# Performance work log

Measured on AMD Instinct MI355X. Metric: run time of the kernel, lower is better.

## Reference

```python
import jax, jax.numpy as jnp
import numpy as np

B, DIN, H, DOUT = 4096, 2048, 4096, 2048


def setup_inputs() -> dict:
    key = jax.random.key(0)
    ks = jax.random.split(key, 17)
    x = jax.random.normal(ks[0], (B, DIN), dtype=jnp.float32)
    W0 = jax.random.randint(ks[1], (H, DIN), -127, 128, dtype=jnp.int32)
    b0 = jax.random.randint(ks[2], (H,), -127, 128, dtype=jnp.int32)
    W2 = jax.random.randint(ks[3], (H, H), -127, 128, dtype=jnp.int32)
    b2 = jax.random.randint(ks[4], (H,), -127, 128, dtype=jnp.int32)
    W4 = jax.random.randint(ks[5], (DOUT, H), -127, 128, dtype=jnp.int32)
    b4 = jax.random.randint(ks[6], (DOUT,), -127, 128, dtype=jnp.int32)
    # amax scalars: positive calibration ranges in [0.5, 2.0)
    amaxes = [jax.random.uniform(ks[7 + i], (), jnp.float32, 0.5, 2.0) for i in range(9)]
    (a0_in, a0_w, a0_b, a2_in, a2_w, a2_b, a4_in, a4_w, a4_b) = amaxes
    return {"x": x, "W0": W0, "b0": b0, "W2": W2, "b2": b2, "W4": W4, "b4": b4,
            "a0_in": a0_in, "a0_w": a0_w, "a0_b": a0_b,
            "a2_in": a2_in, "a2_w": a2_w, "a2_b": a2_b,
            "a4_in": a4_in, "a4_w": a4_w, "a4_b": a4_b}


def _quant(x, amax):
    # torch: clamp(round(x * 127/amax), -127, 127).int()
    scale = 127.0 / amax
    return jnp.clip(jnp.round(x * scale), -127.0, 127.0).astype(jnp.int32)


def _layer(x, W, b, a_in, a_w, a_b):
    xq = _quant(x, a_in)                                      # [B, in] int32
    acc = jnp.matmul(xq, W.T, preferred_element_type=jnp.int32)  # [B, out] int32
    y = acc.astype(jnp.float32) * (a_w * a_in / (127.0 ** 2))    # double dequant
    return y + b.astype(jnp.float32) * (a_b / 127.0)             # single dequant bias


def reference(x, W0, b0, W2, b2, W4, b4,
              a0_in, a0_w, a0_b, a2_in, a2_w, a2_b, a4_in, a4_w, a4_b):
    x = x.reshape(x.shape[0], -1)
    x = _layer(x, W0, b0, a0_in, a0_w, a0_b)
    x = jax.nn.relu(x)
    x = _layer(x, W2, b2, a2_in, a2_w, a2_b)
    x = jax.nn.relu(x)
    x = _layer(x, W4, b4, a4_in, a4_w, a4_b)
    return x
```

## Files before the change

kernel.cpp:

```cpp
#include <hip/hip_runtime.h>

using i32x4 = __attribute__((ext_vector_type(4))) int;

#define DEVI static __device__ __forceinline__

DEVI void gload_lds16(const void* g, void* l) {
  __builtin_amdgcn_global_load_lds(
      (const __attribute__((address_space(1))) void*)g,
      (__attribute__((address_space(3))) void*)l, 16, 0, 0);
}

template <int N> DEVI void vmcnt_n() {
  asm volatile("s_waitcnt vmcnt(%0)" ::"n"(N) : "memory");
}
template <int N> DEVI void lgkm_n() {
  asm volatile("s_waitcnt lgkmcnt(%0)" ::"n"(N) : "memory");
}

#define FENCE() asm volatile("" ::: "memory")
#define BARX()                    \
  do {                            \
    FENCE();                      \
    __builtin_amdgcn_s_barrier(); \
    FENCE();                      \
  } while (0)
#define SCHB() __builtin_amdgcn_sched_barrier(0)
#define PRIO1() __builtin_amdgcn_s_setprio(1)
#define PRIO0() __builtin_amdgcn_s_setprio(0)

__global__ void __launch_bounds__(256) pack_w_kernel(const int* __restrict__ w,
                                                     signed char* __restrict__ o,
                                                     int n4) {
  int stride = gridDim.x * blockDim.x;
  for (int i = blockIdx.x * blockDim.x + threadIdx.x; i < n4; i += stride) {
    int4 v = reinterpret_cast<const int4*>(w)[i];
    char4 c;
    c.x = (signed char)v.x;
    c.y = (signed char)v.y;
    c.z = (signed char)v.z;
    c.w = (signed char)v.w;
    reinterpret_cast<char4*>(o)[i] = c;
  }
}

__global__ void __launch_bounds__(256) quant_x_kernel(const float* __restrict__ x,
                                                      signed char* __restrict__ o,
                                                      const float* __restrict__ amax,
                                                      int n4) {
  const float s = 127.0f / amax[0];
  int stride = gridDim.x * blockDim.x;
  for (int i = blockIdx.x * blockDim.x + threadIdx.x; i < n4; i += stride) {
    float4 v = reinterpret_cast<const float4*>(x)[i];
    char4 c;
    float q;
    q = fminf(fmaxf(rintf(__fmul_rn(v.x, s)), -127.0f), 127.0f); c.x = (signed char)(int)q;
    q = fminf(fmaxf(rintf(__fmul_rn(v.y, s)), -127.0f), 127.0f); c.y = (signed char)(int)q;
    q = fminf(fmaxf(rintf(__fmul_rn(v.z, s)), -127.0f), 127.0f); c.z = (signed char)(int)q;
    q = fminf(fmaxf(rintf(__fmul_rn(v.w, s)), -127.0f), 127.0f); c.w = (signed char)(int)q;
    reinterpret_cast<char4*>(o)[i] = c;
  }
}


#define GB(b, j, k0_)                                           \
  gload_lds16(Wb + (size_t)((j)*64 + srow) * K + (k0_),         \
              &lds[b][ABYTES + (j)*8192 + tid * 16])
#define GA(b, r0, k0_)                                          \
  gload_lds16(Ab + (size_t)((r0) + srow) * K + (k0_),           \
              &lds[b][(r0)*128 + tid * 16])

#define STG_B_EARLY(b, kt)                                              \
  do {                                                                  \
    const int k0_ = (kt)*128 + scol;                                    \
    _Pragma("unroll") for (int j = 0; j < NBE; ++j) GB(b, j, k0_);      \
  } while (0)
#define STG_B_LATE(b, kt)                                               \
  do {                                                                  \
    const int k0_ = (kt)*128 + scol;                                    \
    _Pragma("unroll") for (int j = NBE; j < NN; ++j) GB(b, j, k0_);     \
  } while (0)
#define STG_A01(b, kt)               \
  do {                               \
    const int k0_ = (kt)*128 + scol; \
    GA(b, 0, k0_);                   \
    GA(b, 128, k0_);                 \
  } while (0)
#define STG_A23(b, kt)               \
  do {                               \
    const int k0_ = (kt)*128 + scol; \
    GA(b, 64, k0_);                  \
    GA(b, 192, k0_);                 \
  } while (0)

#define AF_(b, m, h) \
  (*(const i32x4*)&lds[b][(wrl + (m)*16 + ro) * 128 + ((h) ? cS1 : cS0)])
#define BF_(b, n, h) \
  (*(const i32x4*)&lds[b][ABYTES + (wcl + (n)*16 + ro) * 128 + ((h) ? cS1 : cS0)])

#define RD_AF(dst, b, m0)            \
  do {                               \
    dst[0][0] = AF_(b, m0, 0);       \
    dst[0][1] = AF_(b, m0, 1);       \
    dst[1][0] = AF_(b, (m0) + 1, 0); \
    dst[1][1] = AF_(b, (m0) + 1, 1); \
  } while (0)

#define READ_BF(b)                                   \
  do {                                               \
    _Pragma("unroll") for (int n = 0; n < NN; ++n) { \
      bf[n][0] = BF_(b, n, 0);                       \
      bf[n][1] = BF_(b, n, 1);                       \
    }                                                \
  } while (0)

#define MFMA_P(mp, af)                                                                     \
  do {                                                                                     \
    _Pragma("unroll") for (int n = 0; n < NN; ++n) {                                       \
      acc[2 * (mp)][n] =                                                                   \
          __builtin_amdgcn_mfma_i32_16x16x64_i8(af[0][0], bf[n][0], acc[2 * (mp)][n], 0, 0, 0); \
      acc[2 * (mp)][n] =                                                                   \
          __builtin_amdgcn_mfma_i32_16x16x64_i8(af[0][1], bf[n][1], acc[2 * (mp)][n], 0, 0, 0); \
      acc[2 * (mp) + 1][n] = __builtin_amdgcn_mfma_i32_16x16x64_i8(                        \
          af[1][0], bf[n][0], acc[2 * (mp) + 1][n], 0, 0, 0);                              \
      acc[2 * (mp) + 1][n] = __builtin_amdgcn_mfma_i32_16x16x64_i8(                        \
          af[1][1], bf[n][1], acc[2 * (mp) + 1][n], 0, 0, 0);                              \
    }                                                                                      \
  } while (0)

#define TILE_STEADY(b, t)                       \
  do {                                          \
    READ_BF(b);                                 \
    RD_AF(afB, b, 2);                           \
    STG_B_LATE(1 - (b), (t) + 1);               \
    STG_A01(1 - (b), (t) + 1);                  \
    vmcnt_n<NN + 2>();                          \
    BARX(); lgkm_n<4>(); SCHB();                \
    PRIO1(); MFMA_P(0, afA); PRIO0();           \
    RD_AF(afA, b, 4);                           \
    STG_A23(1 - (b), (t) + 1);                  \
    BARX(); lgkm_n<4>(); SCHB();                \
    PRIO1(); MFMA_P(1, afB); PRIO0();           \
    RD_AF(afB, b, 6);                           \
    vmcnt_n<2>();                               \
    BARX(); lgkm_n<4>(); SCHB();                \
    PRIO1(); MFMA_P(2, afA); PRIO0();           \
    RD_AF(afA, 1 - (b), 0);                     \
    if ((t) + 2 < nt) STG_B_EARLY(b, (t) + 2);  \
    BARX(); lgkm_n<4>(); SCHB();                \
    PRIO1(); MFMA_P(3, afB); PRIO0();           \
  } while (0)

#define TILE_LAST(b)                            \
  do {                                          \
    READ_BF(b);                                 \
    RD_AF(afB, b, 2);                           \
    vmcnt_n<0>();                               \
    BARX(); lgkm_n<4>(); SCHB();                \
    PRIO1(); MFMA_P(0, afA); PRIO0();           \
    RD_AF(afA, b, 4);                           \
    BARX(); lgkm_n<4>(); SCHB();                \
    PRIO1(); MFMA_P(1, afB); PRIO0();           \
    RD_AF(afB, b, 6);                           \
    BARX(); lgkm_n<4>(); SCHB();                \
    PRIO1(); MFMA_P(2, afA); PRIO0();           \
    BARX(); lgkm_n<0>(); SCHB();                \
    PRIO1(); MFMA_P(3, afB); PRIO0();           \
  } while (0)

template <int BN, int OUT_I8>
__global__ __launch_bounds__(512, 2) void gemm8_kernel(
    const signed char* __restrict__ A, const signed char* __restrict__ W,
    const int* __restrict__ bias, void* __restrict__ out, int M, int N, int K,
    const float* __restrict__ p_ain, const float* __restrict__ p_aw,
    const float* __restrict__ p_ab, const float* __restrict__ p_anext) {
  static_assert(BN == 256 || BN == 128, "");
  constexpr int NN = BN / 64;
  constexpr int NBE = NN / 2;
  constexpr int ABYTES = 256 * 128;
  __shared__ signed char lds[2][ABYTES + BN * 128];

  const int tid = threadIdx.x;
  const int lane = tid & 63;
  const int wave = tid >> 6;
  const int wrl = (wave >> 2) * 128;
  const int wcl = (wave & 3) * (BN / 4);
  const int tileM = blockIdx.y * 256;
  const int tileN = blockIdx.x * BN;

  const signed char* Ab = A + (size_t)tileM * K;
  const signed char* Wb = W + (size_t)tileN * K;

  const int srow = tid >> 3;
  const int scol = ((tid & 7) ^ (srow & 7)) * 16;

  const int ro = lane & 15;
  const int kg = lane >> 4;
  const int cS0 = ((kg ^ (ro & 7)) << 4);
  const int cS1 = (((4 + kg) ^ (ro & 7)) << 4);

  const int nt = K >> 7;

  i32x4 acc[8][NN] = {};
  i32x4 afA[2][2], afB[2][2], bf[NN][2];

  {
    const int k0_ = scol;
#pragma unroll
    for (int j = 0; j < NN; ++j) GB(0, j, k0_);
    GA(0, 0, k0_);
    GA(0, 128, k0_);
    GA(0, 64, k0_);
    GA(0, 192, k0_);
  }
  FENCE();
  STG_B_EARLY(1, 1);
  vmcnt_n<NBE>();
  BARX();
  RD_AF(afA, 0, 0);

  for (int t = 0; t < nt - 2; t += 2) {
    TILE_STEADY(0, t);
    TILE_STEADY(1, t + 1);
  }
  TILE_STEADY(0, nt - 2);
  TILE_LAST(1);

  const float s1 = __fmul_rn(p_aw[0], p_ain[0]) / 16129.0f;
  const float s2 = p_ab[0] / 127.0f;
  float qs = 0.0f;
  if (OUT_I8) qs = 127.0f / p_anext[0];

#pragma unroll
  for (int m = 0; m < 8; ++m) {
#pragma unroll
    for (int n = 0; n < NN; ++n) {
      const int col = tileN + wcl + n * 16 + ro;
      const int row0 = tileM + wrl + m * 16 + kg * 4;
      const float bv = __fmul_rn((float)bias[col], s2);
#pragma unroll
      for (int i = 0; i < 4; ++i) {
        float y = __fadd_rn(__fmul_rn((float)acc[m][n][i], s1), bv);
        if (OUT_I8) {
          float rl = fmaxf(y, 0.0f);
          float q = fminf(rintf(__fmul_rn(rl, qs)), 127.0f);
          ((signed char*)out)[(size_t)(row0 + i) * N + col] = (signed char)(int)q;
        } else {
          ((float*)out)[(size_t)(row0 + i) * N + col] = y;
        }
      }
    }
  }
}

extern "C" void kernel_launch(void* const* d_in, const int* in_sizes, int n_in,
                              void* d_out, int out_size, void* d_ws, size_t ws_size,
                              hipStream_t stream) {
  const float* x = (const float*)d_in[0];
  const int* W0 = (const int*)d_in[1];
  const int* b0 = (const int*)d_in[2];
  const int* W2 = (const int*)d_in[3];
  const int* b2 = (const int*)d_in[4];
  const int* W4 = (const int*)d_in[5];
  const int* b4 = (const int*)d_in[6];
  const float* a0_in = (const float*)d_in[7];
  const float* a0_w = (const float*)d_in[8];
  const float* a0_b = (const float*)d_in[9];
  const float* a2_in = (const float*)d_in[10];
  const float* a2_w = (const float*)d_in[11];
  const float* a2_b = (const float*)d_in[12];
  const float* a4_in = (const float*)d_in[13];
  const float* a4_w = (const float*)d_in[14];
  const float* a4_b = (const float*)d_in[15];

  constexpr int Bb = 4096, DIN = 2048, H = 4096, DOUT = 2048;
  constexpr size_t MB = 1u << 20;

  char* ws = (char*)d_ws;
  signed char* xq0 = (signed char*)(ws);
  signed char* xq2 = (signed char*)(ws);
  signed char* W0q = (signed char*)(ws + 8 * MB);
  signed char* W2q = (signed char*)(ws + 16 * MB);
  signed char* W4q = (signed char*)(ws + 32 * MB);
  signed char* xq1 = (signed char*)(ws + 40 * MB);

  pack_w_kernel<<<2048, 256, 0, stream>>>(W0, W0q, H * DIN / 4);
  pack_w_kernel<<<2048, 256, 0, stream>>>(W2, W2q, H * H / 4);
  pack_w_kernel<<<2048, 256, 0, stream>>>(W4, W4q, DOUT * H / 4);
  quant_x_kernel<<<2048, 256, 0, stream>>>(x, xq0, a0_in, Bb * DIN / 4);

  gemm8_kernel<256, 1><<<dim3(H / 256, Bb / 256), 512, 0, stream>>>(
      xq0, W0q, b0, xq1, Bb, H, DIN, a0_in, a0_w, a0_b, a2_in);
  gemm8_kernel<256, 1><<<dim3(H / 256, Bb / 256), 512, 0, stream>>>(
      xq1, W2q, b2, xq2, Bb, H, H, a2_in, a2_w, a2_b, a4_in);
  gemm8_kernel<128, 0><<<dim3(DOUT / 128, Bb / 256), 512, 0, stream>>>(
      xq2, W4q, b4, d_out, Bb, DOUT, H, a4_in, a4_w, a4_b, a4_in);
}
```

Measured before the change: 166.4 us.

## Fuse prep kernels, add XCD-aware tile swizzle, and extra barriers around MFMA phases

Merges the three weight-pack kernels and the input-quantize kernel into one launch, with 4-way unrolled loops and packed int stores, to cut launch overhead. Remaps block IDs so consecutive tiles land on the same XCD (8-way round-robin), aiming for better L2 reuse of A and W. Adds extra workgroup barriers after each MFMA phase in the GEMM pipeline, which tightens wave lockstep but may add stall time.

```diff
diff --git a/kernel.cpp b/kernel.cpp
--- a/kernel.cpp
+++ b/kernel.cpp
@@ -28,36 +28,77 @@
 #define PRIO1() __builtin_amdgcn_s_setprio(1)
 #define PRIO0() __builtin_amdgcn_s_setprio(0)
 
-__global__ void __launch_bounds__(256) pack_w_kernel(const int* __restrict__ w,
-                                                     signed char* __restrict__ o,
-                                                     int n4) {
-  int stride = gridDim.x * blockDim.x;
-  for (int i = blockIdx.x * blockDim.x + threadIdx.x; i < n4; i += stride) {
-    int4 v = reinterpret_cast<const int4*>(w)[i];
-    char4 c;
-    c.x = (signed char)v.x;
-    c.y = (signed char)v.y;
-    c.z = (signed char)v.z;
-    c.w = (signed char)v.w;
-    reinterpret_cast<char4*>(o)[i] = c;
-  }
-}
-
-__global__ void __launch_bounds__(256) quant_x_kernel(const float* __restrict__ x,
-                                                      signed char* __restrict__ o,
-                                                      const float* __restrict__ amax,
-                                                      int n4) {
-  const float s = 127.0f / amax[0];
-  int stride = gridDim.x * blockDim.x;
-  for (int i = blockIdx.x * blockDim.x + threadIdx.x; i < n4; i += stride) {
-    float4 v = reinterpret_cast<const float4*>(x)[i];
-    char4 c;
-    float q;
-    q = fminf(fmaxf(rintf(__fmul_rn(v.x, s)), -127.0f), 127.0f); c.x = (signed char)(int)q;
-    q = fminf(fmaxf(rintf(__fmul_rn(v.y, s)), -127.0f), 127.0f); c.y = (signed char)(int)q;
-    q = fminf(fmaxf(rintf(__fmul_rn(v.z, s)), -127.0f), 127.0f); c.z = (signed char)(int)q;
-    q = fminf(fmaxf(rintf(__fmul_rn(v.w, s)), -127.0f), 127.0f); c.w = (signed char)(int)q;
-    reinterpret_cast<char4*>(o)[i] = c;
+DEVI int pack4(int4 v) {
+  return (v.x & 255) | ((v.y & 255) << 8) | ((v.z & 255) << 16) | (v.w << 24);
+}
+
+DEVI int quant4(float4 v, float s) {
+  float q;
+  int r;
+  q = fminf(fmaxf(rintf(__fmul_rn(v.x, s)), -127.0f), 127.0f);
+  r = (int)q & 255;
+  q = fminf(fmaxf(rintf(__fmul_rn(v.y, s)), -127.0f), 127.0f);
+  r |= ((int)q & 255) << 8;
+  q = fminf(fmaxf(rintf(__fmul_rn(v.z, s)), -127.0f), 127.0f);
+  r |= ((int)q & 255) << 16;
+  q = fminf(fmaxf(rintf(__fmul_rn(v.w, s)), -127.0f), 127.0f);
+  r |= ((int)q & 255) << 24;
+  return r;
+}
+
+__global__ void __launch_bounds__(256) prep_kernel(
+    const int* __restrict__ W0, const int* __restrict__ W2,
+    const int* __restrict__ W4, const float* __restrict__ x,
+    const float* __restrict__ amax, signed char* __restrict__ W0q,
+    signed char* __restrict__ W2q, signed char* __restrict__ W4q,
+    signed char* __restrict__ xq, int n0, int n2, int n4, int nx,
+    int s0, int s2, int s4, int sx) {
+  const int bid = blockIdx.x;
+  const int tid = threadIdx.x;
+  if (bid < s0 + s2 + s4) {
+    const int* w;
+    signed char* o;
+    int n, lb, nb;
+    if (bid < s0) {
+      w = W0; o = W0q; n = n0; lb = bid; nb = s0;
+    } else if (bid < s0 + s2) {
+      w = W2; o = W2q; n = n2; lb = bid - s0; nb = s2;
+    } else {
+      w = W4; o = W4q; n = n4; lb = bid - s0 - s2; nb = s4;
+    }
+    const int4* __restrict__ src = (const int4*)w;
+    int* __restrict__ dst = (int*)o;
+    const int T = nb * 256;
+    int i = lb * 256 + tid;
+    for (; i + 3 * T < n; i += 4 * T) {
+      int4 a = src[i];
+      int4 b = src[i + T];
+      int4 c = src[i + 2 * T];
+      int4 d = src[i + 3 * T];
+      dst[i] = pack4(a);
+      dst[i + T] = pack4(b);
+      dst[i + 2 * T] = pack4(c);
+      dst[i + 3 * T] = pack4(d);
+    }
+    for (; i < n; i += T) dst[i] = pack4(src[i]);
+  } else {
+    const float s = 127.0f / amax[0];
+    const int lb = bid - s0 - s2 - s4;
+    const float4* __restrict__ src = (const float4*)x;
+    int* __restrict__ dst = (int*)xq;
+    const int T = sx * 256;
+    int i = lb * 256 + tid;
+    for (; i + 3 * T < nx; i += 4 * T) {
+      float4 a = src[i];
+      float4 b = src[i + T];
+      float4 c = src[i + 2 * T];
+      float4 d = src[i + 3 * T];
+      dst[i] = quant4(a, s);
+      dst[i + T] = quant4(b, s);
+      dst[i + 2 * T] = quant4(c, s);
+      dst[i + 3 * T] = quant4(d, s);
+    }
+    for (; i < nx; i += T) dst[i] = quant4(src[i], s);
   }
 }
 
@@ -136,18 +177,22 @@
     vmcnt_n<NN + 2>();                          \
     BARX(); lgkm_n<4>(); SCHB();                \
     PRIO1(); MFMA_P(0, afA); PRIO0();           \
+    BARX();                                     \
     RD_AF(afA, b, 4);                           \
     STG_A23(1 - (b), (t) + 1);                  \
     BARX(); lgkm_n<4>(); SCHB();                \
     PRIO1(); MFMA_P(1, afB); PRIO0();           \
+    BARX();                                     \
     RD_AF(afB, b, 6);                           \
     vmcnt_n<2>();                               \
     BARX(); lgkm_n<4>(); SCHB();                \
     PRIO1(); MFMA_P(2, afA); PRIO0();           \
+    BARX();                                     \
     RD_AF(afA, 1 - (b), 0);                     \
     if ((t) + 2 < nt) STG_B_EARLY(b, (t) + 2);  \
     BARX(); lgkm_n<4>(); SCHB();                \
     PRIO1(); MFMA_P(3, afB); PRIO0();           \
+    BARX();                                     \
   } while (0)
 
 #define TILE_LAST(b)                            \
@@ -157,18 +202,21 @@
     vmcnt_n<0>();                               \
     BARX(); lgkm_n<4>(); SCHB();                \
     PRIO1(); MFMA_P(0, afA); PRIO0();           \
+    BARX();                                     \
     RD_AF(afA, b, 4);                           \
     BARX(); lgkm_n<4>(); SCHB();                \
     PRIO1(); MFMA_P(1, afB); PRIO0();           \
+    BARX();                                     \
     RD_AF(afB, b, 6);                           \
     BARX(); lgkm_n<4>(); SCHB();                \
     PRIO1(); MFMA_P(2, afA); PRIO0();           \
+    BARX();                                     \
     BARX(); lgkm_n<0>(); SCHB();                \
     PRIO1(); MFMA_P(3, afB); PRIO0();           \
   } while (0)
 
 template <int BN, int OUT_I8>
-__global__ __launch_bounds__(512, 2) void gemm8_kernel(
+__global__ __launch_bounds__(512, 2) void gemm_r16_kernel(
     const signed char* __restrict__ A, const signed char* __restrict__ W,
     const int* __restrict__ bias, void* __restrict__ out, int M, int N, int K,
     const float* __restrict__ p_ain, const float* __restrict__ p_aw,
@@ -184,8 +232,12 @@
   const int wave = tid >> 6;
   const int wrl = (wave >> 2) * 128;
   const int wcl = (wave & 3) * (BN / 4);
-  const int tileM = blockIdx.y * 256;
-  const int tileN = blockIdx.x * BN;
+
+  const int lin = blockIdx.y * gridDim.x + blockIdx.x;
+  const int cpx = (gridDim.x * gridDim.y) >> 3;
+  const int swz = (lin & 7) * cpx + (lin >> 3);
+  const int tileM = (swz / gridDim.x) * 256;
+  const int tileN = (swz % gridDim.x) * BN;
 
   const signed char* Ab = A + (size_t)tileM * K;
   const signed char* Wb = W + (size_t)tileN * K;
@@ -283,15 +335,16 @@
   signed char* W4q = (signed char*)(ws + 32 * MB);
   signed char* xq1 = (signed char*)(ws + 40 * MB);
 
-  pack_w_kernel<<<2048, 256, 0, stream>>>(W0, W0q, H * DIN / 4);
-  pack_w_kernel<<<2048, 256, 0, stream>>>(W2, W2q, H * H / 4);
-  pack_w_kernel<<<2048, 256, 0, stream>>>(W4, W4q, DOUT * H / 4);
-  quant_x_kernel<<<2048, 256, 0, stream>>>(x, xq0, a0_in, Bb * DIN / 4);
-
-  gemm8_kernel<256, 1><<<dim3(H / 256, Bb / 256), 512, 0, stream>>>(
+  const int n0 = H * DIN / 4, n2 = H * H / 4, n4 = DOUT * H / 4;
+  const int nx = Bb * DIN / 4;
+  const int s0 = 512, s2 = 1024, s4 = 512, sx = 512;
+  prep_kernel<<<s0 + s2 + s4 + sx, 256, 0, stream>>>(
+      W0, W2, W4, x, a0_in, W0q, W2q, W4q, xq0, n0, n2, n4, nx, s0, s2, s4, sx);
+
+  gemm_r16_kernel<256, 1><<<dim3(H / 256, Bb / 256), 512, 0, stream>>>(
       xq0, W0q, b0, xq1, Bb, H, DIN, a0_in, a0_w, a0_b, a2_in);
-  gemm8_kernel<256, 1><<<dim3(H / 256, Bb / 256), 512, 0, stream>>>(
+  gemm_r16_kernel<256, 1><<<dim3(H / 256, Bb / 256), 512, 0, stream>>>(
       xq1, W2q, b2, xq2, Bb, H, H, a2_in, a2_w, a2_b, a4_in);
-  gemm8_kernel<128, 0><<<dim3(DOUT / 128, Bb / 256), 512, 0, stream>>>(
+  gemm_r16_kernel<128, 0><<<dim3(DOUT / 128, Bb / 256), 512, 0, stream>>>(
       xq2, W4q, b4, d_out, Bb, DOUT, H, a4_in, a4_w, a4_b, a4_in);
 }
```

New measurement: 167.2 us. No clear change (+0.5%).
